# Kernel optimization log

Measured on AMD Instinct MI355X. Metric: run time of the kernel, lower is better.

The kernel has to match this reference:

```python
import jax, jax.numpy as jnp
import numpy as np
import math

N_HEAD, HEAD_DIM = 12, 64
TAU = 1.0


def setup_inputs() -> dict:
    key = jax.random.key(0)
    ks = jax.random.split(key, 4)
    B, T, C = 2, 2048, 768
    x = jax.random.normal(ks[0], (B, T, C), jnp.float32)
    # Linear params (stored as [in, out]; math-equivalent to torch's x @ W.T + b).
    # 0.02 init scale keeps attention logits in a realistic range.
    w_attn = jax.random.normal(ks[1], (C, 3 * N_HEAD * HEAD_DIM), jnp.float32) * 0.02
    b_attn = jnp.zeros((3 * N_HEAD * HEAD_DIM,), jnp.float32)
    w_proj = jax.random.normal(ks[2], (N_HEAD * HEAD_DIM, C), jnp.float32) * 0.02
    b_proj = jnp.zeros((C,), jnp.float32)
    return {"x": x, "w_attn": w_attn, "b_attn": b_attn, "w_proj": w_proj, "b_proj": b_proj}


def reference(x, w_attn, b_attn, w_proj, b_proj):
    B, T, C = x.shape
    nh, hd, tau = N_HEAD, HEAD_DIM, TAU

    qkv = x @ w_attn + b_attn                              # [B,T,3*nh*hd]
    q, k, v = jnp.split(qkv, 3, axis=2)
    to_heads = lambda t: t.reshape(B, T, nh, hd).transpose(0, 2, 1, 3)  # [B,nh,T,hd]
    q, k, v = to_heads(q), to_heads(k), to_heads(v)

    att = jnp.einsum('bhqd,bhkd->bhqk', q, k) * (1.0 / math.sqrt(hd))   # [B,nh,T,T]
    causal = jnp.tril(jnp.ones((T, T), bool))
    att = jnp.where(causal, att, -jnp.inf)

    # Memory-penalty built from head 0 scores.
    S = jax.nn.relu(att[:, 0])                             # [B,T,T]; relu(-inf)=0
    col = jnp.arange(T)
    keep = (col[None, :] != 0) & (col[:, None] != col[None, :])  # zero col 0 and diagonal
    S = S * keep
    # roll rows down by 1 with row 0 zeroed
    S_shifted = jnp.concatenate([jnp.zeros((B, 1, T), S.dtype), S[:, :-1]], axis=1)
    FF = jnp.cumsum(S_shifted, axis=-2)[:, None]           # [B,1,T,T]
    FF_sum = jnp.clip(FF, 0.0, tau).sum(axis=-1)           # [B,1,T]
    positions = jnp.arange(T, dtype=x.dtype).reshape(1, 1, T, 1)
    M = positions - FF_sum / tau                           # broadcasts to [1,B,T,T] (as torch does)

    att = jax.nn.softmax(att - FF, axis=-1)
    y = jnp.einsum('bhqk,bhkd->bhqd', att, v)              # [B,nh,T,hd]
    y = y.transpose(0, 2, 1, 3).reshape(B, T, nh * hd)
    y = y @ w_proj + b_proj
    return (y, M)
```

## Files before the change

### kernel.cpp

```cpp
#include <hip/hip_runtime.h>
#include <cstddef>

#define TT 2048
#define BB 2
#define CC 768
#define NH 12
#define HD 64
#define N3 2304
#define Y_ELEMS (BB*TT*CC)
#define M_ELEMS (BB*TT*TT)

typedef __attribute__((ext_vector_type(8))) short bf16x8;
typedef __attribute__((ext_vector_type(4))) float f32x4;

__device__ inline unsigned short f2b(float f) {
  union { float f; unsigned u; } v; v.f = f;
  unsigned r = (v.u + 0x7FFFu + ((v.u >> 16) & 1u)) >> 16;
  return (unsigned short)r;
}
__device__ inline float b2f(unsigned short u) {
  union { unsigned u; float f; } v; v.u = (unsigned)u << 16; return v.f;
}

__device__ inline void gload_lds16(const unsigned short* g, unsigned short* l) {
  __builtin_amdgcn_global_load_lds(
      (const __attribute__((address_space(1))) unsigned int*)g,
      (__attribute__((address_space(3))) unsigned int*)l, 16, 0, 0);
}

__global__ __launch_bounds__(256) void prep_fused(
    const float* __restrict__ x, const float* __restrict__ w_attn,
    const float* __restrict__ w_proj, const float* __restrict__ b_attn,
    unsigned short* __restrict__ xb, unsigned short* __restrict__ wbT,
    unsigned short* __restrict__ wpT,
    float* __restrict__ q0, float* __restrict__ k0) {
  int bid = blockIdx.x;
  int tid = threadIdx.x;
  if (bid < 256) {
    __shared__ float As[16][32];
    __shared__ float Bs[16][64];
    int sec = bid >> 7;
    int mt = bid & 127;
    const float* Bw = w_attn + sec * CC;
    float* Out = sec ? k0 : q0;
    int tx = tid & 15, ty = tid >> 4;
    int m0 = mt * 32;

    int arow = tid >> 3;
    int acol2 = (tid & 7) << 1;
    int brow = tid >> 4;
    int bcol4 = (tid & 15) << 2;

    const float* Aptr = x + (size_t)(m0 + arow) * CC + acol2;
    const float* Bptr = Bw + (size_t)brow * N3 + bcol4;

    float acc[2][4] = {};
    for (int k0_ = 0; k0_ < CC; k0_ += 16) {
      float2 av = *(const float2*)(Aptr + k0_);
      float4 bv = *(const float4*)(Bptr + (size_t)k0_ * N3);
      As[acol2 + 0][arow] = av.x;
      As[acol2 + 1][arow] = av.y;
      *(float4*)&Bs[brow][bcol4] = bv;
      __syncthreads();
#pragma unroll
      for (int kk = 0; kk < 16; ++kk) {
        float2 a2 = *(const float2*)&As[kk][ty << 1];
        float4 b4 = *(const float4*)&Bs[kk][tx << 2];
        float a[2] = {a2.x, a2.y};
        float b[4] = {b4.x, b4.y, b4.z, b4.w};
#pragma unroll
        for (int ii = 0; ii < 2; ++ii)
#pragma unroll
          for (int jj = 0; jj < 4; ++jj) acc[ii][jj] += a[ii] * b[jj];
      }
      __syncthreads();
    }
    float4 bv = *(const float4*)(b_attn + sec * CC + (tx << 2));
#pragma unroll
    for (int ii = 0; ii < 2; ++ii) {
      int m = m0 + (ty << 1) + ii;
      float4 o;
      o.x = acc[ii][0] + bv.x;
      o.y = acc[ii][1] + bv.y;
      o.z = acc[ii][2] + bv.z;
      o.w = acc[ii][3] + bv.w;
      *(float4*)(Out + (size_t)m * HD + (tx << 2)) = o;
    }
    return;
  }
  if (bid < 1792) {
    size_t i = ((size_t)(bid - 256) * 256 + tid) * 8;
    float4 a = *(const float4*)(x + i);
    float4 b = *(const float4*)(x + i + 4);
    ushort4 o0, o1;
    o0.x = f2b(a.x); o0.y = f2b(a.y); o0.z = f2b(a.z); o0.w = f2b(a.w);
    o1.x = f2b(b.x); o1.y = f2b(b.y); o1.z = f2b(b.z); o1.w = f2b(b.w);
    *(ushort4*)(xb + i) = o0;
    *(ushort4*)(xb + i + 4) = o1;
    return;
  }
  const float* W;
  unsigned short* WT;
  int N, kt, nt;
  if (bid < 2224) {
    int t = bid - 1792;
    W = w_attn; WT = wbT; N = N3;
    kt = t % 12; nt = t / 12;
  } else {
    int t = bid - 2224;
    W = w_proj; WT = wpT; N = CC;
    kt = t % 12; nt = t / 12;
  }
  __shared__ float tile[64][65];
  int r = tid >> 4, c4 = (tid & 15) << 2;
#pragma unroll
  for (int rep = 0; rep < 4; ++rep) {
    int row = rep * 16 + r;
    float4 v = *(const float4*)(W + (size_t)(kt * 64 + row) * N + nt * 64 + c4);
    tile[row][c4 + 0] = v.x; tile[row][c4 + 1] = v.y;
    tile[row][c4 + 2] = v.z; tile[row][c4 + 3] = v.w;
  }
  __syncthreads();
#pragma unroll
  for (int rep = 0; rep < 4; ++rep) {
    int nrow = rep * 16 + r;
    ushort4 o;
    o.x = f2b(tile[c4 + 0][nrow]); o.y = f2b(tile[c4 + 1][nrow]);
    o.z = f2b(tile[c4 + 2][nrow]); o.w = f2b(tile[c4 + 3][nrow]);
    *(ushort4*)(WT + (size_t)(nt * 64 + nrow) * CC + kt * 64 + c4) = o;
  }
}

__global__ __launch_bounds__(256, 3) void gemm_qkv_bf16(
    const unsigned short* __restrict__ xb, const unsigned short* __restrict__ wbT,
    const float* __restrict__ b_attn,
    unsigned short* __restrict__ Qb, unsigned short* __restrict__ Kb,
    unsigned short* __restrict__ Vt) {
  __shared__ __align__(16) unsigned short smem_u[17408];
  unsigned short (*Alds)[128][32] = (unsigned short(*)[128][32])smem_u;
  unsigned short (*Blds)[128][32] = (unsigned short(*)[128][32])(smem_u + 8192);
  unsigned short (*Vlds)[136]     = (unsigned short(*)[136])smem_u;

  int mt = blockIdx.x, nt = blockIdx.y;
  int sec = nt / 6, h0 = (nt % 6) * 2;
  int wave = threadIdx.x >> 6, lane = threadIdx.x & 63;
  int lr = lane & 15, lg = lane >> 4;
  int m0 = mt * 128;
  int n0 = nt * 128;

  int srow = lane >> 2;
  int sslot = (lane & 3) ^ (srow & 3);

#define STAGE_AB(BUF, K0)                                                       \
  {                                                                             \
    _Pragma("unroll")                                                           \
    for (int p = 0; p < 2; ++p) {                                               \
      int ar = wave * 32 + p * 16 + srow;                                       \
      gload_lds16(xb + (size_t)(m0 + ar) * CC + (K0) + (sslot << 3),            \
                  &Alds[BUF][wave * 32 + p * 16][0]);                           \
      gload_lds16(wbT + (size_t)(n0 + ar) * CC + (K0) + (sslot << 3),           \
                  &Blds[BUF][wave * 32 + p * 16][0]);                           \
    }                                                                           \
  }

  f32x4 acc[2][8];
#pragma unroll
  for (int mi = 0; mi < 2; ++mi)
#pragma unroll
    for (int nj = 0; nj < 8; ++nj) acc[mi][nj] = (f32x4){0.f, 0.f, 0.f, 0.f};

  STAGE_AB(0, 0)
  __syncthreads();

  int fslot = lg ^ (lr & 3);
  for (int kt = 0; kt < 24; ++kt) {
    int cur = kt & 1;
    if (kt < 23) STAGE_AB(cur ^ 1, (kt + 1) * 32)
    bf16x8 af[2], bf[8];
#pragma unroll
    for (int mi = 0; mi < 2; ++mi)
      af[mi] = *(const bf16x8*)&Alds[cur][wave * 32 + mi * 16 + lr][fslot << 3];
#pragma unroll
    for (int nj = 0; nj < 8; ++nj)
      bf[nj] = *(const bf16x8*)&Blds[cur][nj * 16 + lr][fslot << 3];
    __builtin_amdgcn_s_setprio(1);
#pragma unroll
    for (int nj = 0; nj < 8; ++nj)
#pragma unroll
      for (int mi = 0; mi < 2; ++mi)
        acc[mi][nj] = __builtin_amdgcn_mfma_f32_16x16x32_bf16(af[mi], bf[nj], acc[mi][nj], 0, 0, 0);
    __builtin_amdgcn_s_setprio(0);
    __syncthreads();
  }
#undef STAGE_AB

  int b = m0 >> 11;
  float bias[8];
#pragma unroll
  for (int nj = 0; nj < 8; ++nj) bias[nj] = b_attn[n0 + nj * 16 + lr];

  if (sec < 2) {
    float qscale = (sec == 0) ? 0.125f : 1.0f;
    unsigned short* OutB = (sec == 0 ? Qb : Kb);
    int tbase = (m0 & 2047) + wave * 32 + lg * 4;
#pragma unroll
    for (int nj = 0; nj < 8; ++nj) {
      int h = h0 + (nj >> 2);
      int d = (nj & 3) * 16 + lr;
      unsigned short* Out = OutB + (size_t)(b * NH + h) * TT * HD;
#pragma unroll
      for (int mi = 0; mi < 2; ++mi)
#pragma unroll
        for (int r = 0; r < 4; ++r) {
          int t = tbase + mi * 16 + r;
          Out[(size_t)t * HD + d] = f2b((acc[mi][nj][r] + bias[nj]) * qscale);
        }
    }
  } else {
    int tl = wave * 32 + lg * 4;
#pragma unroll
    for (int mi = 0; mi < 2; ++mi)
#pragma unroll
      for (int r = 0; r < 4; ++r)
#pragma unroll
        for (int nj = 0; nj < 8; ++nj)
          Vlds[tl + mi * 16 + r][nj * 16 + lr] = f2b(acc[mi][nj][r] + bias[nj]);
    __syncthreads();
    int d = threadIdx.x & 63, tc = threadIdx.x >> 6;
    int tblk = (m0 & 2047);
#pragma unroll
    for (int hh = 0; hh < 2; ++hh) {
      unsigned short* Ov = Vt + ((size_t)(b * NH + h0 + hh) * HD + d) * TT + tblk + tc * 32;
      int c = hh * 64 + d;
#pragma unroll
      for (int i8 = 0; i8 < 4; ++i8) {
        ushort4 o0, o1;
        o0.x = Vlds[tc * 32 + i8 * 8 + 0][c]; o0.y = Vlds[tc * 32 + i8 * 8 + 1][c];
        o0.z = Vlds[tc * 32 + i8 * 8 + 2][c]; o0.w = Vlds[tc * 32 + i8 * 8 + 3][c];
        o1.x = Vlds[tc * 32 + i8 * 8 + 4][c]; o1.y = Vlds[tc * 32 + i8 * 8 + 5][c];
        o1.z = Vlds[tc * 32 + i8 * 8 + 6][c]; o1.w = Vlds[tc * 32 + i8 * 8 + 7][c];
        *(ushort4*)(Ov + i8 * 8) = o0;
        *(ushort4*)(Ov + i8 * 8 + 4) = o1;
      }
    }
  }
}

__global__ __launch_bounds__(256) void score0_kernel(
    const float* __restrict__ q0, const float* __restrict__ k0,
    float* __restrict__ Sbuf, float* __restrict__ partials) {
  int it = blockIdx.x, jt = blockIdx.y, b = blockIdx.z;
  int tid = threadIdx.x;
  int i0 = it * 64, j0 = jt * 64;
  if (jt > it) {
    if (tid < 64) partials[((size_t)(b * 32 + it)) * TT + j0 + tid] = 0.f;
    return;
  }
  __shared__ float Qs[64][64];
  __shared__ float Ks[64][64];
  int row = tid >> 2;
  int dq = (tid & 3) << 2;
  const float* qb = q0 + (size_t)((b * TT) + i0 + row) * HD;
  const float* kb = k0 + (size_t)((b * TT) + j0 + row) * HD;
#pragma unroll
  for (int rep = 0; rep < 4; ++rep) {
    int d = dq + rep * 16;
    float4 qv = *(const float4*)(qb + d);
    float4 kv = *(const float4*)(kb + d);
    Qs[d + 0][row] = qv.x; Qs[d + 1][row] = qv.y;
    Qs[d + 2][row] = qv.z; Qs[d + 3][row] = qv.w;
    Ks[d + 0][row] = kv.x; Ks[d + 1][row] = kv.y;
    Ks[d + 2][row] = kv.z; Ks[d + 3][row] = kv.w;
  }
  __syncthreads();
  int tx = tid & 15, ty = tid >> 4;
  float acc[4][4] = {};
#pragma unroll 8
  for (int kk = 0; kk < 64; ++kk) {
    float4 a4 = *(const float4*)&Qs[kk][ty << 2];
    float4 b4 = *(const float4*)&Ks[kk][tx << 2];
    float a[4] = {a4.x, a4.y, a4.z, a4.w};
    float b[4] = {b4.x, b4.y, b4.z, b4.w};
#pragma unroll
    for (int ii = 0; ii < 4; ++ii)
#pragma unroll
      for (int jj = 0; jj < 4; ++jj) acc[ii][jj] += a[ii] * b[jj];
  }
  float red4[4] = {0.f, 0.f, 0.f, 0.f};
#pragma unroll
  for (int ii = 0; ii < 4; ++ii) {
    int r = i0 + (ty << 2) + ii;
    int gi = (b * TT) + r;
    float ov[4];
#pragma unroll
    for (int jj = 0; jj < 4; ++jj) {
      ov[jj] = fmaxf(acc[ii][jj] * 0.125f, 0.f);
      int j = j0 + (tx << 2) + jj;
      if (j >= 1 && j < r) red4[jj] += ov[jj];
    }
    float4 o; o.x = ov[0]; o.y = ov[1]; o.z = ov[2]; o.w = ov[3];
    *(float4*)(Sbuf + (size_t)gi * TT + j0 + (tx << 2)) = o;
  }
  __syncthreads();
  *(float4*)&Qs[ty][tx << 2] = *(float4*)red4;
  __syncthreads();
  if (tid < 64) {
    float cs = 0.f;
#pragma unroll
    for (int t = 0; t < 16; ++t) cs += Qs[t][tid];
    partials[((size_t)(b * 32 + it)) * TT + j0 + tid] = cs;
  }
}

__global__ __launch_bounds__(256) void scan_write(
    const float* __restrict__ Sbuf, const float* __restrict__ partials,
    unsigned short* __restrict__ Eb, float* __restrict__ ffpart) {
  int j = blockIdx.x * 256 + threadIdx.x;
  int chunk = blockIdx.y, b = blockIdx.z;
  float run = 0.f;
  for (int c = 0; c < chunk; ++c) run += partials[((size_t)(b * 32 + c)) * TT + j];
  int r0 = chunk * 64;
  int jswz = (j & ~63) | ((j & 15) << 2) | ((j >> 4) & 3);
  const float* base = Sbuf + (size_t)(b * TT + r0) * TT + j;
  unsigned short* ebase = Eb + (size_t)(b * TT + r0) * TT + jswz;
  __shared__ float wsum[4][64];
  int wv = threadIdx.x >> 6;
  for (int rb = 0; rb < 64; rb += 8) {
    float v[8];
#pragma unroll
    for (int u = 0; u < 8; ++u) {
      int r = r0 + rb + u;
      v[u] = (j >= 1 && j < r) ? base[(size_t)(rb + u) * TT] : 0.f;
    }
#pragma unroll
    for (int u = 0; u < 8; ++u) {
      int rr = rb + u;
      ebase[(size_t)rr * TT] = f2b(__expf(-run));
      float c1 = fminf(run, 1.f);
#pragma unroll
      for (int o = 1; o < 64; o <<= 1) c1 += __shfl_xor(c1, o);
      if ((threadIdx.x & 63) == 0) wsum[wv][rr] = c1;
      run += v[u];
    }
  }
  __syncthreads();
  if (threadIdx.x < 64)
    ffpart[((size_t)(b * 8) + blockIdx.x) * TT + r0 + threadIdx.x] =
        wsum[0][threadIdx.x] + wsum[1][threadIdx.x] +
        wsum[2][threadIdx.x] + wsum[3][threadIdx.x];
}

__global__ __launch_bounds__(256, 3) void attn_mfma(
    const unsigned short* __restrict__ Qb, const unsigned short* __restrict__ Kb,
    const unsigned short* __restrict__ Vt, const unsigned short* __restrict__ Eb,
    unsigned short* __restrict__ yhb) {
  int xbh = blockIdx.x;
  int b = (xbh >> 2) & 1;
  int h = ((xbh >> 3) << 2) | (xbh & 3);
  int yy = blockIdx.y;
  int g4 = (yy & 1) ? (yy >> 1) : (31 - (yy >> 1));
  int wave = threadIdx.x >> 6, lane = threadIdx.x & 63;
  int lr = lane & 15, lg = lane >> 4;
  int i0 = g4 * 64 + wave * 16;
  int bh = b * NH + h;
  const unsigned short* Qh = Qb + (size_t)bh * TT * HD;
  const unsigned short* Kh = Kb + (size_t)bh * TT * HD;
  const unsigned short* Vh = Vt + (size_t)bh * HD * TT;
  const unsigned short* Erow = Eb + ((size_t)(b * TT) + i0 + lg * 4) * TT + 4 * lr;

  __shared__ __align__(16) unsigned short Ksh[2][64][64];
  __shared__ __align__(16) unsigned short Vsh[2][64][64];
  __shared__ __align__(16) unsigned short Plds[4][16][80];

  int rowoff = lane >> 3;
  int sslot  = (lane & 7) ^ rowoff;

  bf16x8 qf[2];
#pragma unroll
  for (int ks = 0; ks < 2; ++ks)
    qf[ks] = *(const bf16x8*)(Qh + (size_t)(i0 + lr) * HD + ks * 32 + lg * 8);

  f32x4 acc[4];
  float lrun[4] = {0.f, 0.f, 0.f, 0.f};
#pragma unroll
  for (int q = 0; q < 4; ++q) acc[q] = (f32x4){0.f, 0.f, 0.f, 0.f};

#define STAGE_KV(BUF, J0)                                                      \
  {                                                                            \
    _Pragma("unroll")                                                          \
    for (int p = 0; p < 2; ++p) {                                              \
      int r0 = wave * 16 + p * 8;                                              \
      gload_lds16(Kh + (size_t)((J0) + r0 + rowoff) * HD + sslot * 8,          \
                  &Ksh[BUF][r0][0]);                                           \
      gload_lds16(Vh + (size_t)(r0 + rowoff) * TT + (J0) + sslot * 8,          \
                  &Vsh[BUF][r0][0]);                                           \
    }                                                                          \
  }

  STAGE_KV(0, 0)
  __syncthreads();

  for (int kt = 0; kt <= g4; ++kt) {
    int cur = kt & 1;
    int j0 = kt * 64;
    if (kt < g4) STAGE_KV(cur ^ 1, j0 + 64)

    ushort4 ev[4];
#pragma unroll
    for (int r = 0; r < 4; ++r)
      ev[r] = *(const ushort4*)(Erow + (size_t)r * TT + j0);

    f32x4 s[4];
    __builtin_amdgcn_s_setprio(1);
#pragma unroll
    for (int nj = 0; nj < 4; ++nj) {
      int row = nj * 16 + lr;
      int sw = row & 7;
      bf16x8 k0f = *(const bf16x8*)&Ksh[cur][row][(lg ^ sw) << 3];
      bf16x8 k1f = *(const bf16x8*)&Ksh[cur][row][((4 + lg) ^ sw) << 3];
      f32x4 z = (f32x4){0.f, 0.f, 0.f, 0.f};
      z = __builtin_amdgcn_mfma_f32_16x16x32_bf16(qf[0], k0f, z, 0, 0, 0);
      s[nj] = __builtin_amdgcn_mfma_f32_16x16x32_bf16(qf[1], k1f, z, 0, 0, 0);
    }
    __builtin_amdgcn_s_setprio(0);

    int ibase = i0 + lg * 4;
    if (kt == g4) {
#pragma unroll
      for (int nj = 0; nj < 4; ++nj)
#pragma unroll
        for (int r = 0; r < 4; ++r)
          if (j0 + nj * 16 + lr > ibase + r) s[nj][r] = -1e30f;
    }

#pragma unroll
    for (int r = 0; r < 4; ++r) {
      float p0 = b2f(ev[r].x) * __expf(s[0][r]);
      float p1 = b2f(ev[r].y) * __expf(s[1][r]);
      float p2 = b2f(ev[r].z) * __expf(s[2][r]);
      float p3 = b2f(ev[r].w) * __expf(s[3][r]);
      lrun[r] += (p0 + p1) + (p2 + p3);
      Plds[wave][lg * 4 + r][0 * 16 + lr] = f2b(p0);
      Plds[wave][lg * 4 + r][1 * 16 + lr] = f2b(p1);
      Plds[wave][lg * 4 + r][2 * 16 + lr] = f2b(p2);
      Plds[wave][lg * 4 + r][3 * 16 + lr] = f2b(p3);
    }

    bf16x8 pa0 = *(const bf16x8*)&Plds[wave][lr][lg * 8];
    bf16x8 pa1 = *(const bf16x8*)&Plds[wave][lr][32 + lg * 8];
    __builtin_amdgcn_s_setprio(1);
#pragma unroll
    for (int nd = 0; nd < 4; ++nd) {
      int row = nd * 16 + lr;
      int sw = row & 7;
      bf16x8 v0f = *(const bf16x8*)&Vsh[cur][row][(lg ^ sw) << 3];
      bf16x8 v1f = *(const bf16x8*)&Vsh[cur][row][((4 + lg) ^ sw) << 3];
      acc[nd] = __builtin_amdgcn_mfma_f32_16x16x32_bf16(pa0, v0f, acc[nd], 0, 0, 0);
      acc[nd] = __builtin_amdgcn_mfma_f32_16x16x32_bf16(pa1, v1f, acc[nd], 0, 0, 0);
    }
    __builtin_amdgcn_s_setprio(0);

    __syncthreads();
  }
#undef STAGE_KV

#pragma unroll
  for (int r = 0; r < 4; ++r) {
    lrun[r] += __shfl_xor(lrun[r], 1);
    lrun[r] += __shfl_xor(lrun[r], 2);
    lrun[r] += __shfl_xor(lrun[r], 4);
    lrun[r] += __shfl_xor(lrun[r], 8);
    float inv = 1.f / lrun[r];
    int ig = i0 + lg * 4 + r;
    unsigned short* ob = yhb + (size_t)(b * TT + ig) * CC + h * HD;
#pragma unroll
    for (int nd = 0; nd < 4; ++nd)
      ob[nd * 16 + lr] = f2b(acc[nd][r] * inv);
  }
}

__global__ __launch_bounds__(256, 3) void proj_m_fused(
    const unsigned short* __restrict__ yhb, const unsigned short* __restrict__ wpT,
    const float* __restrict__ b_proj, float* __restrict__ y,
    const float* __restrict__ ffpart, float* __restrict__ Mout) {
  int bid = blockIdx.x;
  if (bid >= 192) {
    int idx4 = (bid - 192) * 256 + threadIdx.x;
    int stride = (gridDim.x - 192) * 256;
    for (; idx4 < M_ELEMS / 4; idx4 += stride) {
      int idx = idx4 << 2;
      int j = idx & (TT - 1);
      int i = (idx >> 11) & (TT - 1);
      int b = idx >> 22;
      const float* fp = ffpart + ((size_t)(b * 8)) * TT + j;
      float4 s = make_float4(0.f, 0.f, 0.f, 0.f);
#pragma unroll
      for (int p = 0; p < 8; ++p) {
        float4 v = *(const float4*)(fp + (size_t)p * TT);
        s.x += v.x; s.y += v.y; s.z += v.z; s.w += v.w;
      }
      float fi = (float)i;
      float4 o = make_float4(fi - s.x, fi - s.y, fi - s.z, fi - s.w);
      *(float4*)(Mout + idx) = o;
    }
    return;
  }
  __shared__ __align__(16) unsigned short Alds[2][128][32];
  __shared__ __align__(16) unsigned short Blds[2][128][32];
  int mt = bid & 31, nt = bid >> 5;
  int wave = threadIdx.x >> 6, lane = threadIdx.x & 63;
  int lr = lane & 15, lg = lane >> 4;
  int m0 = mt * 128;
  int n0 = nt * 128;

  int srow = lane >> 2;
  int sslot = (lane & 3) ^ (srow & 3);

#define STAGE_AB(BUF, K0)                                                       \
  {                                                                             \
    _Pragma("unroll")                                                           \
    for (int p = 0; p < 2; ++p) {                                               \
      int ar = wave * 32 + p * 16 + srow;                                       \
      gload_lds16(yhb + (size_t)(m0 + ar) * CC + (K0) + (sslot << 3),           \
                  &Alds[BUF][wave * 32 + p * 16][0]);                           \
      gload_lds16(wpT + (size_t)(n0 + ar) * CC + (K0) + (sslot << 3),           \
                  &Blds[BUF][wave * 32 + p * 16][0]);                           \
    }                                                                           \
  }

  f32x4 acc[2][8];
#pragma unroll
  for (int mi = 0; mi < 2; ++mi)
#pragma unroll
    for (int nj = 0; nj < 8; ++nj) acc[mi][nj] = (f32x4){0.f, 0.f, 0.f, 0.f};

  STAGE_AB(0, 0)
  __syncthreads();

  int fslot = lg ^ (lr & 3);
  for (int kt = 0; kt < 24; ++kt) {
    int cur = kt & 1;
    if (kt < 23) STAGE_AB(cur ^ 1, (kt + 1) * 32)
    bf16x8 af[2], bf[8];
#pragma unroll
    for (int mi = 0; mi < 2; ++mi)
      af[mi] = *(const bf16x8*)&Alds[cur][wave * 32 + mi * 16 + lr][fslot << 3];
#pragma unroll
    for (int nj = 0; nj < 8; ++nj)
      bf[nj] = *(const bf16x8*)&Blds[cur][nj * 16 + lr][fslot << 3];
    __builtin_amdgcn_s_setprio(1);
#pragma unroll
    for (int nj = 0; nj < 8; ++nj)
#pragma unroll
      for (int mi = 0; mi < 2; ++mi)
        acc[mi][nj] = __builtin_amdgcn_mfma_f32_16x16x32_bf16(af[mi], bf[nj], acc[mi][nj], 0, 0, 0);
    __builtin_amdgcn_s_setprio(0);
    __syncthreads();
  }
#undef STAGE_AB

  float bias[8];
#pragma unroll
  for (int nj = 0; nj < 8; ++nj) bias[nj] = b_proj[n0 + nj * 16 + lr];
#pragma unroll
  for (int mi = 0; mi < 2; ++mi)
#pragma unroll
    for (int r = 0; r < 4; ++r) {
      int m = m0 + wave * 32 + mi * 16 + lg * 4 + r;
#pragma unroll
      for (int nj = 0; nj < 8; ++nj)
        y[(size_t)m * CC + n0 + nj * 16 + lr] = acc[mi][nj][r] + bias[nj];
    }
}

extern "C" void kernel_launch(void* const* d_in, const int* in_sizes, int n_in,
                              void* d_out, int out_size, void* d_ws, size_t ws_size,
                              hipStream_t stream) {
  const float* x      = (const float*)d_in[0];
  const float* w_attn = (const float*)d_in[1];
  const float* b_attn = (const float*)d_in[2];
  const float* w_proj = (const float*)d_in[3];
  const float* b_proj = (const float*)d_in[4];

  float* y    = (float*)d_out;
  float* Mreg = y + Y_ELEMS;

  float* ws = (float*)d_ws;
  float* q0       = ws;
  float* k0       = q0 + (size_t)BB * TT * HD;
  float* partials = k0 + (size_t)BB * TT * HD;
  float* ffpart   = partials + (size_t)BB * 32 * TT;
  unsigned short* xb  = (unsigned short*)(ffpart + (size_t)BB * 8 * TT);
  unsigned short* wbT = xb + (size_t)Y_ELEMS;
  unsigned short* wpT = wbT + (size_t)N3 * CC;
  unsigned short* Qb  = wpT + (size_t)CC * CC;
  unsigned short* Kb  = Qb + (size_t)BB * NH * TT * HD;
  unsigned short* Vt  = Kb + (size_t)BB * NH * TT * HD;
  unsigned short* yhb = Vt + (size_t)BB * NH * TT * HD;
  unsigned short* Eb  = yhb + (size_t)Y_ELEMS;

  prep_fused<<<2368, 256, 0, stream>>>(x, w_attn, w_proj, b_attn,
                                       xb, wbT, wpT, q0, k0);
  gemm_qkv_bf16<<<dim3(32, 18), 256, 0, stream>>>(xb, wbT, b_attn, Qb, Kb, Vt);
  score0_kernel<<<dim3(32, 32, BB), 256, 0, stream>>>(q0, k0, Mreg, partials);
  scan_write<<<dim3(8, 32, BB), 256, 0, stream>>>(Mreg, partials, Eb, ffpart);
  attn_mfma<<<dim3(24, 32), 256, 0, stream>>>(Qb, Kb, Vt, Eb, yhb);
  proj_m_fused<<<1216, 256, 0, stream>>>(yhb, wpT, b_proj, y, ffpart, Mreg);
}
```

Measured before the change: 170.3 us.

## Fuse head-0 score kernel into QKV GEMM launch and skip upper-triangle scan blocks

The head-0 score kernel becomes extra blocks inside the QKV GEMM launch, dispatched by block index with the shared-memory buffer reused. This removes one kernel launch and lets the small score tiles overlap with GEMM tiles. The scan kernel now returns early for column blocks entirely above the causal diagonal, writing only zeroed ffpart entries. This skips the Eb writes and Sbuf reads there, which is correct only if later kernels never read Eb in the masked region.

```diff
diff --git a/kernel.cpp b/kernel.cpp
--- a/kernel.cpp
+++ b/kernel.cpp
@@ -131,17 +131,89 @@
   }
 }
 
-__global__ __launch_bounds__(256, 3) void gemm_qkv_bf16(
+__global__ __launch_bounds__(256, 3) void gemm_score_fused(
     const unsigned short* __restrict__ xb, const unsigned short* __restrict__ wbT,
     const float* __restrict__ b_attn,
     unsigned short* __restrict__ Qb, unsigned short* __restrict__ Kb,
-    unsigned short* __restrict__ Vt) {
+    unsigned short* __restrict__ Vt,
+    const float* __restrict__ q0, const float* __restrict__ k0,
+    float* __restrict__ Sbuf, float* __restrict__ partials) {
   __shared__ __align__(16) unsigned short smem_u[17408];
+  int bid = blockIdx.x;
+  int tid = threadIdx.x;
+
+  if (bid >= 576) {
+    int t = bid - 576;
+    int b = t >> 10;
+    int rem = t & 1023;
+    int it = rem >> 5, jt = rem & 31;
+    int i0 = it * 64, j0 = jt * 64;
+    if (jt > it) {
+      if (tid < 64) partials[((size_t)(b * 32 + it)) * TT + j0 + tid] = 0.f;
+      return;
+    }
+    float (*Qs)[64] = (float(*)[64])smem_u;
+    float (*Ks)[64] = (float(*)[64])(smem_u + 8192);
+    int row = tid >> 2;
+    int dq = (tid & 3) << 2;
+    const float* qb = q0 + (size_t)((b * TT) + i0 + row) * HD;
+    const float* kb = k0 + (size_t)((b * TT) + j0 + row) * HD;
+#pragma unroll
+    for (int rep = 0; rep < 4; ++rep) {
+      int d = dq + rep * 16;
+      float4 qv = *(const float4*)(qb + d);
+      float4 kv = *(const float4*)(kb + d);
+      Qs[d + 0][row] = qv.x; Qs[d + 1][row] = qv.y;
+      Qs[d + 2][row] = qv.z; Qs[d + 3][row] = qv.w;
+      Ks[d + 0][row] = kv.x; Ks[d + 1][row] = kv.y;
+      Ks[d + 2][row] = kv.z; Ks[d + 3][row] = kv.w;
+    }
+    __syncthreads();
+    int tx = tid & 15, ty = tid >> 4;
+    float acc[4][4] = {};
+#pragma unroll 8
+    for (int kk = 0; kk < 64; ++kk) {
+      float4 a4 = *(const float4*)&Qs[kk][ty << 2];
+      float4 b4 = *(const float4*)&Ks[kk][tx << 2];
+      float a[4] = {a4.x, a4.y, a4.z, a4.w};
+      float bb[4] = {b4.x, b4.y, b4.z, b4.w};
+#pragma unroll
+      for (int ii = 0; ii < 4; ++ii)
+#pragma unroll
+        for (int jj = 0; jj < 4; ++jj) acc[ii][jj] += a[ii] * bb[jj];
+    }
+    float red4[4] = {0.f, 0.f, 0.f, 0.f};
+#pragma unroll
+    for (int ii = 0; ii < 4; ++ii) {
+      int r = i0 + (ty << 2) + ii;
+      int gi = (b * TT) + r;
+      float ov[4];
+#pragma unroll
+      for (int jj = 0; jj < 4; ++jj) {
+        ov[jj] = fmaxf(acc[ii][jj] * 0.125f, 0.f);
+        int j = j0 + (tx << 2) + jj;
+        if (j >= 1 && j < r) red4[jj] += ov[jj];
+      }
+      float4 o; o.x = ov[0]; o.y = ov[1]; o.z = ov[2]; o.w = ov[3];
+      *(float4*)(Sbuf + (size_t)gi * TT + j0 + (tx << 2)) = o;
+    }
+    __syncthreads();
+    *(float4*)&Qs[ty][tx << 2] = *(float4*)red4;
+    __syncthreads();
+    if (tid < 64) {
+      float cs = 0.f;
+#pragma unroll
+      for (int t2 = 0; t2 < 16; ++t2) cs += Qs[t2][tid];
+      partials[((size_t)(b * 32 + it)) * TT + j0 + tid] = cs;
+    }
+    return;
+  }
+
   unsigned short (*Alds)[128][32] = (unsigned short(*)[128][32])smem_u;
   unsigned short (*Blds)[128][32] = (unsigned short(*)[128][32])(smem_u + 8192);
   unsigned short (*Vlds)[136]     = (unsigned short(*)[136])smem_u;
 
-  int mt = blockIdx.x, nt = blockIdx.y;
+  int mt = bid & 31, nt = bid >> 5;
   int sec = nt / 6, h0 = (nt % 6) * 2;
   int wave = threadIdx.x >> 6, lane = threadIdx.x & 63;
   int lr = lane & 15, lg = lane >> 4;
@@ -246,80 +318,20 @@
   }
 }
 
-__global__ __launch_bounds__(256) void score0_kernel(
-    const float* __restrict__ q0, const float* __restrict__ k0,
-    float* __restrict__ Sbuf, float* __restrict__ partials) {
-  int it = blockIdx.x, jt = blockIdx.y, b = blockIdx.z;
-  int tid = threadIdx.x;
-  int i0 = it * 64, j0 = jt * 64;
-  if (jt > it) {
-    if (tid < 64) partials[((size_t)(b * 32 + it)) * TT + j0 + tid] = 0.f;
-    return;
-  }
-  __shared__ float Qs[64][64];
-  __shared__ float Ks[64][64];
-  int row = tid >> 2;
-  int dq = (tid & 3) << 2;
-  const float* qb = q0 + (size_t)((b * TT) + i0 + row) * HD;
-  const float* kb = k0 + (size_t)((b * TT) + j0 + row) * HD;
-#pragma unroll
-  for (int rep = 0; rep < 4; ++rep) {
-    int d = dq + rep * 16;
-    float4 qv = *(const float4*)(qb + d);
-    float4 kv = *(const float4*)(kb + d);
-    Qs[d + 0][row] = qv.x; Qs[d + 1][row] = qv.y;
-    Qs[d + 2][row] = qv.z; Qs[d + 3][row] = qv.w;
-    Ks[d + 0][row] = kv.x; Ks[d + 1][row] = kv.y;
-    Ks[d + 2][row] = kv.z; Ks[d + 3][row] = kv.w;
-  }
-  __syncthreads();
-  int tx = tid & 15, ty = tid >> 4;
-  float acc[4][4] = {};
-#pragma unroll 8
-  for (int kk = 0; kk < 64; ++kk) {
-    float4 a4 = *(const float4*)&Qs[kk][ty << 2];
-    float4 b4 = *(const float4*)&Ks[kk][tx << 2];
-    float a[4] = {a4.x, a4.y, a4.z, a4.w};
-    float b[4] = {b4.x, b4.y, b4.z, b4.w};
-#pragma unroll
-    for (int ii = 0; ii < 4; ++ii)
-#pragma unroll
-      for (int jj = 0; jj < 4; ++jj) acc[ii][jj] += a[ii] * b[jj];
-  }
-  float red4[4] = {0.f, 0.f, 0.f, 0.f};
-#pragma unroll
-  for (int ii = 0; ii < 4; ++ii) {
-    int r = i0 + (ty << 2) + ii;
-    int gi = (b * TT) + r;
-    float ov[4];
-#pragma unroll
-    for (int jj = 0; jj < 4; ++jj) {
-      ov[jj] = fmaxf(acc[ii][jj] * 0.125f, 0.f);
-      int j = j0 + (tx << 2) + jj;
-      if (j >= 1 && j < r) red4[jj] += ov[jj];
-    }
-    float4 o; o.x = ov[0]; o.y = ov[1]; o.z = ov[2]; o.w = ov[3];
-    *(float4*)(Sbuf + (size_t)gi * TT + j0 + (tx << 2)) = o;
-  }
-  __syncthreads();
-  *(float4*)&Qs[ty][tx << 2] = *(float4*)red4;
-  __syncthreads();
-  if (tid < 64) {
-    float cs = 0.f;
-#pragma unroll
-    for (int t = 0; t < 16; ++t) cs += Qs[t][tid];
-    partials[((size_t)(b * 32 + it)) * TT + j0 + tid] = cs;
-  }
-}
-
 __global__ __launch_bounds__(256) void scan_write(
     const float* __restrict__ Sbuf, const float* __restrict__ partials,
     unsigned short* __restrict__ Eb, float* __restrict__ ffpart) {
-  int j = blockIdx.x * 256 + threadIdx.x;
+  int jb = blockIdx.x;
   int chunk = blockIdx.y, b = blockIdx.z;
+  int r0 = chunk * 64;
+  if (jb * 256 >= r0 + 64) {
+    if (threadIdx.x < 64)
+      ffpart[((size_t)(b * 8) + jb) * TT + r0 + threadIdx.x] = 0.f;
+    return;
+  }
+  int j = jb * 256 + threadIdx.x;
   float run = 0.f;
   for (int c = 0; c < chunk; ++c) run += partials[((size_t)(b * 32 + c)) * TT + j];
-  int r0 = chunk * 64;
   int jswz = (j & ~63) | ((j & 15) << 2) | ((j >> 4) & 3);
   const float* base = Sbuf + (size_t)(b * TT + r0) * TT + j;
   unsigned short* ebase = Eb + (size_t)(b * TT + r0) * TT + jswz;
@@ -345,7 +357,7 @@
   }
   __syncthreads();
   if (threadIdx.x < 64)
-    ffpart[((size_t)(b * 8) + blockIdx.x) * TT + r0 + threadIdx.x] =
+    ffpart[((size_t)(b * 8) + jb) * TT + r0 + threadIdx.x] =
         wsum[0][threadIdx.x] + wsum[1][threadIdx.x] +
         wsum[2][threadIdx.x] + wsum[3][threadIdx.x];
 }
@@ -601,8 +613,8 @@
 
   prep_fused<<<2368, 256, 0, stream>>>(x, w_attn, w_proj, b_attn,
                                        xb, wbT, wpT, q0, k0);
-  gemm_qkv_bf16<<<dim3(32, 18), 256, 0, stream>>>(xb, wbT, b_attn, Qb, Kb, Vt);
-  score0_kernel<<<dim3(32, 32, BB), 256, 0, stream>>>(q0, k0, Mreg, partials);
+  gemm_score_fused<<<2624, 256, 0, stream>>>(
+      xb, wbT, b_attn, Qb, Kb, Vt, q0, k0, Mreg, partials);
   scan_write<<<dim3(8, 32, BB), 256, 0, stream>>>(Mreg, partials, Eb, ffpart);
   attn_mfma<<<dim3(24, 32), 256, 0, stream>>>(Qb, Kb, Vt, Eb, yhb);
   proj_m_fused<<<1216, 256, 0, stream>>>(yhb, wpT, b_proj, y, ffpart, Mreg);
```

Measured after the change: 160.1 us. -6.0%, faster.
